# Performance work log

Measured on AMD Instinct MI355X. Metric: run time of the kernel, lower is better.

Reference implementation:

```python
import jax, jax.numpy as jnp
import numpy as np

N, E, D, C, L = 50000, 800000, 128, 10, 3
TAU = 0.5
EPS = 1e-5


def _ln(h, g, b):
    m = jnp.mean(h, axis=-1, keepdims=True)
    v = jnp.mean((h - m) ** 2, axis=-1, keepdims=True)
    return (h - m) * jax.lax.rsqrt(v + EPS) * g + b


def _gumbel_hard(logits, gnoise, tau):
    # gumbel_softmax(hard=True): straight-through one-hot of softmax((logits+g)/tau)
    y_soft = jax.nn.softmax((logits + gnoise) / tau, axis=-1)
    idx = jnp.argmax(y_soft, axis=-1)
    y_hard = jax.nn.one_hot(idx, logits.shape[-1], dtype=y_soft.dtype)
    return jax.lax.stop_gradient(y_hard - y_soft) + y_soft


def setup_inputs() -> dict:
    key = jax.random.key(0)
    ks = jax.random.split(key, 20)
    s = lambda *sh: 1.0 / np.sqrt(sh[0])
    inp = {
        "x": jax.random.normal(ks[0], (N, D), jnp.float32),
        "edge_index": jax.random.randint(ks[1], (2, E), 0, N, jnp.int64),
        # encoder (node_encoder Linear in_dim->env_dim)
        "W_enc": jax.random.normal(ks[2], (D, D), jnp.float32) * s(D),
        "b_enc": jnp.zeros((D,), jnp.float32),
        # shared hidden LayerNorm
        "ln_g": jnp.ones((D,), jnp.float32),
        "ln_b": jnp.zeros((D,), jnp.float32),
        # env GNN layers (root / neighbor weights + bias), L layers
        "Wr": jax.random.normal(ks[3], (L, D, D), jnp.float32) * s(D),
        "Wn": jax.random.normal(ks[4], (L, D, D), jnp.float32) * s(D),
        "bl": jnp.zeros((L, D), jnp.float32),
        # in/out action nets (1 layer each, env_dim -> 2 logits)
        "Wa_in_r": jax.random.normal(ks[5], (D, 2), jnp.float32) * s(D),
        "Wa_in_n": jax.random.normal(ks[6], (D, 2), jnp.float32) * s(D),
        "ba_in": jnp.zeros((2,), jnp.float32),
        "Wa_out_r": jax.random.normal(ks[7], (D, 2), jnp.float32) * s(D),
        "Wa_out_n": jax.random.normal(ks[8], (D, 2), jnp.float32) * s(D),
        "ba_out": jnp.zeros((2,), jnp.float32),
        # decoder (dec_num_layers=1 -> single Linear env_dim -> num_classes)
        "W_dec": jax.random.normal(ks[9], (D, C), jnp.float32) * s(D),
        "b_dec": jnp.zeros((C,), jnp.float32),
        # pre-sampled Gumbel noise per layer for in/out action gates
        "gin": jax.random.gumbel(ks[10], (L, N, 2), jnp.float32),
        "gout": jax.random.gumbel(ks[11], (L, N, 2), jnp.float32),
    }
    return inp


def reference(x, edge_index, W_enc, b_enc, ln_g, ln_b, Wr, Wn, bl,
              Wa_in_r, Wa_in_n, ba_in, Wa_out_r, Wa_out_n, ba_out,
              W_dec, b_dec, gin, gout):
    u, v = edge_index[0], edge_index[1]
    n = x.shape[0]
    # node encoder + (use_encoders=False) dropout(0)+act
    h = jax.nn.relu(x @ W_enc + b_enc)
    node_states = []
    for l in range(L):
        hn = _ln(h, ln_g, ln_b)
        # unweighted neighbor aggregation shared by both action nets
        agg = jax.ops.segment_sum(hn[u], v, num_segments=n)  # [N, D]
        in_logits = hn @ Wa_in_r + agg @ Wa_in_n + ba_in
        out_logits = hn @ Wa_out_r + agg @ Wa_out_n + ba_out
        in_p = _gumbel_hard(in_logits, gin[l], TAU)
        out_p = _gumbel_hard(out_logits, gout[l], TAU)
        # edge gate: listen prob of target * broadcast prob of source
        ew = in_p[v, 0] * out_p[u, 0]  # [E]
        aggw = jax.ops.segment_sum(ew[:, None] * hn[u], v, num_segments=n)
        out = jax.nn.relu(hn @ Wr[l] + aggw @ Wn[l] + bl[l])
        # node state bookkeeping: 0 standard, 1 broadcast-only, 2 listen-only, 3 isolated
        act = jax.lax.stop_gradient(ew)
        is_b = (jax.ops.segment_max(act, u, num_segments=n) > 0.5).astype(jnp.int32)
        is_l = (jax.ops.segment_max(act, v, num_segments=n) > 0.5).astype(jnp.int32)
        node_states.append(3 - 2 * is_b - is_l)
        h = hn + out  # skip connection (onto the normalized x, as in the source)
    h = _ln(h, ln_g, ln_b)
    result = h @ W_dec + b_dec
    return result, jnp.stack(node_states)
```

## Files before the change

### kernel.cpp

```cpp
#include <hip/hip_runtime.h>

#define DIM 128
#define NCLS 10

__device__ __forceinline__ void gload_lds16(const float4* g, float4* l) {
    __builtin_amdgcn_global_load_lds((const __attribute__((address_space(1))) char*)g,
                                     (__attribute__((address_space(3))) char*)l,
                                     16, 0, 0);
}

__global__ void k_hist(const int* __restrict__ ei, int E, int* __restrict__ deg) {
    int e = blockIdx.x * 256 + threadIdx.x;
    if (e < E) atomicAdd(&deg[ei[E + e]], 1);
}

__global__ void k_scan1(const int* __restrict__ deg, int* __restrict__ row_start,
                        int* __restrict__ bsum, int n) {
    int tid = threadIdx.x;
    int base = blockIdx.x * 1024 + tid * 4;
    int v0 = 0, v1 = 0, v2 = 0, v3 = 0;
    if (base + 3 < n) {
        int4 t = *(const int4*)(deg + base);
        v0 = t.x; v1 = t.y; v2 = t.z; v3 = t.w;
    } else {
        if (base + 0 < n) v0 = deg[base + 0];
        if (base + 1 < n) v1 = deg[base + 1];
        if (base + 2 < n) v2 = deg[base + 2];
        if (base + 3 < n) v3 = deg[base + 3];
    }
    int s = v0 + v1 + v2 + v3;
    int lane = tid & 63, w = tid >> 6;
    int inc = s;
#pragma unroll
    for (int o = 1; o < 64; o <<= 1) {
        int t = __shfl_up(inc, o);
        if (lane >= o) inc += t;
    }
    __shared__ int wsum[4];
    if (lane == 63) wsum[w] = inc;
    __syncthreads();
    int woff = 0;
    for (int i = 0; i < w; i++) woff += wsum[i];
    int run = woff + inc - s;
    if (base + 0 < n) row_start[base + 0] = run; run += v0;
    if (base + 1 < n) row_start[base + 1] = run; run += v1;
    if (base + 2 < n) row_start[base + 2] = run; run += v2;
    if (base + 3 < n) row_start[base + 3] = run;
    if (tid == 0) bsum[blockIdx.x] = wsum[0] + wsum[1] + wsum[2] + wsum[3];
}

__global__ void k_scan2(int* __restrict__ bsum, int nb) {
    int tid = threadIdx.x;
    if (nb <= 64) {
        int v = (tid < nb) ? bsum[tid] : 0;
        int inc = v;
#pragma unroll
        for (int o = 1; o < 64; o <<= 1) {
            int t = __shfl_up(inc, o);
            if (tid >= o) inc += t;
        }
        if (tid < nb) bsum[tid] = inc - v;
    } else if (tid == 0) {
        int acc = 0;
        for (int i = 0; i < nb; i++) { int t = bsum[i]; bsum[i] = acc; acc += t; }
    }
}

__global__ void k_scan3(int* __restrict__ row_start, int* __restrict__ cursor,
                        const int* __restrict__ bsum, int n, int E) {
    int i = blockIdx.x * 256 + threadIdx.x;
    if (i < n) {
        int r = row_start[i] + bsum[i >> 10];
        row_start[i] = r;
        cursor[i] = r;
    }
    if (i == n) row_start[n] = E;
}

__global__ void k_fill(const int* __restrict__ ei, int E, int* __restrict__ cursor,
                       int* __restrict__ csr) {
    int e = blockIdx.x * 256 + threadIdx.x;
    if (e < E) {
        int u = ei[e], v = ei[E + e];
        int pos = atomicAdd(&cursor[v], 1);
        csr[pos] = u;
    }
}

__global__ void k_action(const float* __restrict__ proj, const int* __restrict__ row_start,
                         const int* __restrict__ csr,
                         const float* __restrict__ bain, const float* __restrict__ baon,
                         const float* __restrict__ gin_l, const float* __restrict__ gout_l,
                         int* __restrict__ in_bit, int* __restrict__ out_bit,
                         int* __restrict__ is_b, int n) {
    int v = blockIdx.x * 256 + threadIdx.x;
    if (v >= n) return;
    is_b[v] = 0;
    int b0 = row_start[v], b1 = row_start[v + 1];
    double a0 = 0.0, a1 = 0.0, a2 = 0.0, a3 = 0.0;
    for (int e = b0; e < b1; e++) {
        int u = csr[e];
        float4 p = *(const float4*)(proj + (size_t)u * 8);
        a0 += p.x; a1 += p.y; a2 += p.z; a3 += p.w;
    }
    float4 r = *(const float4*)(proj + (size_t)v * 8 + 4);
    float2 gi = *(const float2*)(gin_l + (size_t)v * 2);
    float2 go = *(const float2*)(gout_l + (size_t)v * 2);
    float li0 = (float)a0 + r.x + bain[0] + gi.x;
    float li1 = (float)a1 + r.y + bain[1] + gi.y;
    float lo0 = (float)a2 + r.z + baon[0] + go.x;
    float lo1 = (float)a3 + r.w + baon[1] + go.y;
    in_bit[v]  = (li0 >= li1) ? 1 : 0;
    out_bit[v] = (lo0 >= lo1) ? 1 : 0;
}

__global__ void k_aggw(const float* __restrict__ hn, const int* __restrict__ row_start,
                       const int* __restrict__ csr, const int* __restrict__ in_bit,
                       const int* __restrict__ out_bit,
                       int* __restrict__ is_b, int* __restrict__ is_l,
                       float* __restrict__ aggw, int n) {
    int wid = (blockIdx.x * 256 + threadIdx.x) >> 6;
    int lane = threadIdx.x & 63;
    if (wid >= n) return;
    int d0 = lane * 2;
    double ax = 0.0, ay = 0.0;
    int anyg = 0;
    if (in_bit[wid]) {
        int base = row_start[wid], end = row_start[wid + 1];
        for (int off = base; off < end; off += 64) {
            int m = min(64, end - off);
            int myu = 0, myb = 0;
            if (lane < m) { myu = csr[off + lane]; myb = out_bit[myu]; }
            unsigned long long mask = __ballot(myb != 0);
            anyg |= (mask != 0ull);
            while (mask) {
                int i = __ffsll((unsigned long long)mask) - 1;
                mask &= mask - 1;
                int u = __shfl(myu, i);
                if (lane == 0) is_b[u] = 1;
                float2 t = *(const float2*)(hn + (size_t)u * DIM + d0);
                ax += t.x; ay += t.y;
            }
        }
    }
    if (lane == 0) is_l[wid] = anyg;
    ((float2*)(aggw + (size_t)wid * DIM))[lane] = make_float2((float)ax, (float)ay);
}

template <int HAS_B, int SKIP, int DO_LN, int DO_PROJ, int DO_STATES, int DO_DEC, int WRITE_H>
__launch_bounds__(256)
__attribute__((amdgpu_waves_per_eu(4, 4)))
__global__ void k_gemm(const float* __restrict__ A, const float* __restrict__ W1,
                       const float* __restrict__ B, const float* __restrict__ W2,
                       const float* __restrict__ bias,
                       const float* __restrict__ ln_g, const float* __restrict__ ln_b,
                       const float* __restrict__ Wain, const float* __restrict__ Waon,
                       const float* __restrict__ Wair, const float* __restrict__ Waor,
                       const int* __restrict__ is_b, const int* __restrict__ is_l,
                       const float* __restrict__ Wdec, const float* __restrict__ bdec,
                       float* __restrict__ out, float* __restrict__ proj,
                       float* __restrict__ states_l, float* __restrict__ dec_out, int n) {
    __shared__ float sW[32][128];
    __shared__ float sA[64][36];
    int tid = threadIdx.x;
    int rowBase = blockIdx.x * 64;
    int ty = tid >> 4, tx = tid & 15;
    int c0 = tx * 4, c1 = 64 + tx * 4;
    float acc[4][8];
#pragma unroll
    for (int i = 0; i < 4; i++)
#pragma unroll
        for (int j = 0; j < 8; j++) acc[i][j] = 0.f;

    for (int p = 0; p < 1 + HAS_B; p++) {
        const float* Ap = p ? B : A;
        const float* Wp = p ? W2 : W1;
        for (int kc = 0; kc < DIM; kc += 32) {
            __syncthreads();
            {
                const float4* src = (const float4*)(Wp + kc * DIM);
                float4* dst = (float4*)(&sW[0][0]);
#pragma unroll
                for (int i = 0; i < 4; i++) {
                    int j = i * 256 + tid;
                    gload_lds16(src + j, dst + j);
                }
            }
            {
#pragma unroll
                for (int i = 0; i < 2; i++) {
                    int j = i * 256 + tid;
                    int r = j >> 3, c4 = (j & 7) * 4;
                    float4 va = (rowBase + r < n)
                        ? *(const float4*)(Ap + (size_t)(rowBase + r) * DIM + kc + c4)
                        : make_float4(0.f, 0.f, 0.f, 0.f);
                    *(float4*)&sA[r][c4] = va;
                }
            }
            __syncthreads();
#pragma unroll
            for (int kk = 0; kk < 32; kk += 4) {
                float4 a[4];
#pragma unroll
                for (int i = 0; i < 4; i++) a[i] = *(const float4*)&sA[i * 16 + ty][kk];
#pragma unroll
                for (int q = 0; q < 4; q++) {
                    float4 w0 = *(const float4*)&sW[kk + q][c0];
                    float4 w1 = *(const float4*)&sW[kk + q][c1];
#pragma unroll
                    for (int i = 0; i < 4; i++) {
                        float av = (&a[i].x)[q];
                        acc[i][0] += av * w0.x;
                        acc[i][1] += av * w0.y;
                        acc[i][2] += av * w0.z;
                        acc[i][3] += av * w0.w;
                        acc[i][4] += av * w1.x;
                        acc[i][5] += av * w1.y;
                        acc[i][6] += av * w1.z;
                        acc[i][7] += av * w1.w;
                    }
                }
            }
        }
    }

    float* sWd = (float*)&sW[0][0];
    if (DO_DEC) {
        __syncthreads();
        for (int i = tid; i < NCLS * DIM; i += 256) {
            int d = i / NCLS, c = i % NCLS;
            sWd[c * DIM + d] = Wdec[i];
        }
        __syncthreads();
    }

    float4 bias0 = *(const float4*)&bias[c0];
    float4 bias1 = *(const float4*)&bias[c1];
    float bv[8] = {bias0.x, bias0.y, bias0.z, bias0.w, bias1.x, bias1.y, bias1.z, bias1.w};
    float gv[8], bbv[8];
    if (DO_LN) {
        float4 g0 = *(const float4*)&ln_g[c0];
        float4 g1 = *(const float4*)&ln_g[c1];
        float4 lb0 = *(const float4*)&ln_b[c0];
        float4 lb1 = *(const float4*)&ln_b[c1];
        gv[0]=g0.x; gv[1]=g0.y; gv[2]=g0.z; gv[3]=g0.w; gv[4]=g1.x; gv[5]=g1.y; gv[6]=g1.z; gv[7]=g1.w;
        bbv[0]=lb0.x; bbv[1]=lb0.y; bbv[2]=lb0.z; bbv[3]=lb0.w; bbv[4]=lb1.x; bbv[5]=lb1.y; bbv[6]=lb1.z; bbv[7]=lb1.w;
    }

#pragma unroll
    for (int i = 0; i < 4; i++) {
        int r = rowBase + i * 16 + ty;
        if (r >= n) continue;
        float v[8];
        if (SKIP) {
            float4 s0 = *(const float4*)(A + (size_t)r * DIM + c0);
            float4 s1 = *(const float4*)(A + (size_t)r * DIM + c1);
            float sv[8] = {s0.x, s0.y, s0.z, s0.w, s1.x, s1.y, s1.z, s1.w};
#pragma unroll
            for (int j = 0; j < 8; j++) v[j] = fmaxf(acc[i][j] + bv[j], 0.f) + sv[j];
        } else {
#pragma unroll
            for (int j = 0; j < 8; j++) v[j] = fmaxf(acc[i][j] + bv[j], 0.f);
        }
        if (DO_LN) {
            float s = 0.f, q = 0.f;
#pragma unroll
            for (int j = 0; j < 8; j++) { s += v[j]; q += v[j] * v[j]; }
#pragma unroll
            for (int o = 1; o < 16; o <<= 1) { s += __shfl_xor(s, o); q += __shfl_xor(q, o); }
            float m = s * (1.f / DIM);
            float var = q * (1.f / DIM) - m * m;
            float inv = rsqrtf(var + 1e-5f);
#pragma unroll
            for (int j = 0; j < 8; j++) v[j] = (v[j] - m) * inv * gv[j] + bbv[j];
        }
        if (WRITE_H) {
            *(float4*)(out + (size_t)r * DIM + c0) = make_float4(v[0], v[1], v[2], v[3]);
            *(float4*)(out + (size_t)r * DIM + c1) = make_float4(v[4], v[5], v[6], v[7]);
        }
        if (DO_STATES) {
            if (tx == 0) states_l[r] = (float)(3 - 2 * is_b[r] - is_l[r]);
        }
        if (DO_PROJ) {
            float pv[8];
            auto dotw = [&](const float* Wm, float& p0, float& p1) {
                float4 q0 = *(const float4*)(Wm + c0 * 2);
                float4 q1 = *(const float4*)(Wm + c0 * 2 + 4);
                float4 q2 = *(const float4*)(Wm + c1 * 2);
                float4 q3 = *(const float4*)(Wm + c1 * 2 + 4);
                p0 = v[0]*q0.x + v[1]*q0.z + v[2]*q1.x + v[3]*q1.z
                   + v[4]*q2.x + v[5]*q2.z + v[6]*q3.x + v[7]*q3.z;
                p1 = v[0]*q0.y + v[1]*q0.w + v[2]*q1.y + v[3]*q1.w
                   + v[4]*q2.y + v[5]*q2.w + v[6]*q3.y + v[7]*q3.w;
            };
            dotw(Wain, pv[0], pv[1]);
            dotw(Waon, pv[2], pv[3]);
            dotw(Wair, pv[4], pv[5]);
            dotw(Waor, pv[6], pv[7]);
#pragma unroll
            for (int o = 1; o < 16; o <<= 1)
#pragma unroll
                for (int j = 0; j < 8; j++) pv[j] += __shfl_xor(pv[j], o);
            if (tx == 0) {
                *(float4*)(proj + (size_t)r * 8)     = make_float4(pv[0], pv[1], pv[2], pv[3]);
                *(float4*)(proj + (size_t)r * 8 + 4) = make_float4(pv[4], pv[5], pv[6], pv[7]);
            }
        }
        if (DO_DEC) {
            float p[NCLS];
#pragma unroll
            for (int c = 0; c < NCLS; c++) {
                float4 wd0 = *(const float4*)&sWd[c * DIM + c0];
                float4 wd1 = *(const float4*)&sWd[c * DIM + c1];
                p[c] = v[0]*wd0.x + v[1]*wd0.y + v[2]*wd0.z + v[3]*wd0.w
                     + v[4]*wd1.x + v[5]*wd1.y + v[6]*wd1.z + v[7]*wd1.w;
            }
#pragma unroll
            for (int o = 1; o < 16; o <<= 1)
#pragma unroll
                for (int c = 0; c < NCLS; c++) p[c] += __shfl_xor(p[c], o);
            if (tx == 0) {
#pragma unroll
                for (int c = 0; c < NCLS; c++) dec_out[(size_t)r * NCLS + c] = p[c] + bdec[c];
            }
        }
    }
}

extern "C" void kernel_launch(void* const* d_in, const int* in_sizes, int n_in,
                              void* d_out, int out_size, void* d_ws, size_t ws_size,
                              hipStream_t stream) {
    const float* x      = (const float*)d_in[0];
    const int*   ei     = (const int*)d_in[1];
    const float* W_enc  = (const float*)d_in[2];
    const float* b_enc  = (const float*)d_in[3];
    const float* ln_g   = (const float*)d_in[4];
    const float* ln_b   = (const float*)d_in[5];
    const float* Wr     = (const float*)d_in[6];
    const float* Wn     = (const float*)d_in[7];
    const float* bl     = (const float*)d_in[8];
    const float* Wair   = (const float*)d_in[9];
    const float* Wain   = (const float*)d_in[10];
    const float* bain   = (const float*)d_in[11];
    const float* Waor   = (const float*)d_in[12];
    const float* Waon   = (const float*)d_in[13];
    const float* baon   = (const float*)d_in[14];
    const float* W_dec  = (const float*)d_in[15];
    const float* b_dec  = (const float*)d_in[16];
    const float* gin    = (const float*)d_in[17];
    const float* gout   = (const float*)d_in[18];

    int n = in_sizes[0] / DIM;
    int E = in_sizes[1] / 2;
    const int L = 3;

    char* wsp = (char*)d_ws;
    auto alloc = [&](size_t bytes) { char* p = wsp; wsp += (bytes + 255) / 256 * 256; return p; };
    float* hn   = (float*)alloc((size_t)n * DIM * 4);
    float* aggw = (float*)alloc((size_t)n * DIM * 4);
    float* proj = (float*)alloc((size_t)n * 8 * 4);
    int* deg       = (int*)alloc((size_t)n * 4);
    int* row_start = (int*)alloc((size_t)(n + 1) * 4);
    int* cursor    = (int*)alloc((size_t)n * 4);
    int* csr       = (int*)alloc((size_t)E * 4);
    int* in_bit    = (int*)alloc((size_t)n * 4);
    int* out_bit   = (int*)alloc((size_t)n * 4);
    int* bsum      = (int*)alloc((size_t)256 * 4);
    int* is_b      = (int*)alloc((size_t)n * 4);
    int* is_l      = (int*)alloc((size_t)n * 4);

    float* out_res    = (float*)d_out;
    float* out_states = out_res + (size_t)n * NCLS;

    int ebl = (E + 255) / 256;
    int nbl = (n + 255) / 256;
    int wbl = (n + 3) / 4;
    int gbl = (n + 63) / 64;
    int nb  = (n + 1023) / 1024;

    hipMemsetAsync(deg, 0, (size_t)n * 4, stream);
    k_hist<<<ebl, 256, 0, stream>>>(ei, E, deg);
    k_scan1<<<nb, 256, 0, stream>>>(deg, row_start, bsum, n);
    k_scan2<<<1, 64, 0, stream>>>(bsum, nb);
    k_scan3<<<(n + 256) / 256, 256, 0, stream>>>(row_start, cursor, bsum, n, E);
    k_fill<<<ebl, 256, 0, stream>>>(ei, E, cursor, csr);

    k_gemm<0, 0, 1, 1, 0, 0, 1><<<gbl, 256, 0, stream>>>(
        x, W_enc, nullptr, nullptr, b_enc, ln_g, ln_b,
        Wain, Waon, Wair, Waor, nullptr, nullptr, nullptr, nullptr,
        hn, proj, nullptr, nullptr, n);

    for (int l = 0; l < L; l++) {
        k_action<<<nbl, 256, 0, stream>>>(proj, row_start, csr, bain, baon,
                                          gin + (size_t)l * n * 2, gout + (size_t)l * n * 2,
                                          in_bit, out_bit, is_b, n);
        k_aggw<<<wbl, 256, 0, stream>>>(hn, row_start, csr, in_bit, out_bit,
                                        is_b, is_l, aggw, n);
        if (l + 1 < L) {
            k_gemm<1, 1, 1, 1, 1, 0, 1><<<gbl, 256, 0, stream>>>(
                hn, Wr + (size_t)l * DIM * DIM, aggw, Wn + (size_t)l * DIM * DIM,
                bl + (size_t)l * DIM, ln_g, ln_b,
                Wain, Waon, Wair, Waor, is_b, is_l, nullptr, nullptr,
                hn, proj, out_states + (size_t)l * n, nullptr, n);
        } else {
            k_gemm<1, 1, 1, 0, 1, 1, 0><<<gbl, 256, 0, stream>>>(
                hn, Wr + (size_t)l * DIM * DIM, aggw, Wn + (size_t)l * DIM * DIM,
                bl + (size_t)l * DIM, ln_g, ln_b,
                Wain, Waon, Wair, Waor, is_b, is_l, W_dec, b_dec,
                hn, nullptr, out_states + (size_t)l * n, out_res, n);
        }
    }
}
```

Before: 481.0 us.

## Overlap root-weight GEMM with weighted neighbor gather in one launch

Splits the per-layer fused GEMM so the hn@Wr product runs in the same launch as the edge-gated neighbor aggregation, with blocks partitioned by index. A follow-up kernel computes aggw@Wn and fuses bias, relu, skip, layernorm, projections and states, reading the stored partial product. The aim is to overlap compute-heavy GEMM blocks with latency-bound gather waves, at the cost of an extra intermediate buffer write and read per layer.

```diff
diff --git a/kernel.cpp b/kernel.cpp
--- a/kernel.cpp
+++ b/kernel.cpp
@@ -114,52 +114,14 @@
     out_bit[v] = (lo0 >= lo1) ? 1 : 0;
 }
 
-__global__ void k_aggw(const float* __restrict__ hn, const int* __restrict__ row_start,
-                       const int* __restrict__ csr, const int* __restrict__ in_bit,
-                       const int* __restrict__ out_bit,
-                       int* __restrict__ is_b, int* __restrict__ is_l,
-                       float* __restrict__ aggw, int n) {
-    int wid = (blockIdx.x * 256 + threadIdx.x) >> 6;
-    int lane = threadIdx.x & 63;
-    if (wid >= n) return;
-    int d0 = lane * 2;
-    double ax = 0.0, ay = 0.0;
-    int anyg = 0;
-    if (in_bit[wid]) {
-        int base = row_start[wid], end = row_start[wid + 1];
-        for (int off = base; off < end; off += 64) {
-            int m = min(64, end - off);
-            int myu = 0, myb = 0;
-            if (lane < m) { myu = csr[off + lane]; myb = out_bit[myu]; }
-            unsigned long long mask = __ballot(myb != 0);
-            anyg |= (mask != 0ull);
-            while (mask) {
-                int i = __ffsll((unsigned long long)mask) - 1;
-                mask &= mask - 1;
-                int u = __shfl(myu, i);
-                if (lane == 0) is_b[u] = 1;
-                float2 t = *(const float2*)(hn + (size_t)u * DIM + d0);
-                ax += t.x; ay += t.y;
-            }
-        }
-    }
-    if (lane == 0) is_l[wid] = anyg;
-    ((float2*)(aggw + (size_t)wid * DIM))[lane] = make_float2((float)ax, (float)ay);
-}
-
-template <int HAS_B, int SKIP, int DO_LN, int DO_PROJ, int DO_STATES, int DO_DEC, int WRITE_H>
 __launch_bounds__(256)
 __attribute__((amdgpu_waves_per_eu(4, 4)))
-__global__ void k_gemm(const float* __restrict__ A, const float* __restrict__ W1,
-                       const float* __restrict__ B, const float* __restrict__ W2,
+__global__ void k_genc(const float* __restrict__ A, const float* __restrict__ W,
                        const float* __restrict__ bias,
                        const float* __restrict__ ln_g, const float* __restrict__ ln_b,
                        const float* __restrict__ Wain, const float* __restrict__ Waon,
                        const float* __restrict__ Wair, const float* __restrict__ Waor,
-                       const int* __restrict__ is_b, const int* __restrict__ is_l,
-                       const float* __restrict__ Wdec, const float* __restrict__ bdec,
-                       float* __restrict__ out, float* __restrict__ proj,
-                       float* __restrict__ states_l, float* __restrict__ dec_out, int n) {
+                       float* __restrict__ out, float* __restrict__ proj, int n) {
     __shared__ float sW[32][128];
     __shared__ float sA[64][36];
     int tid = threadIdx.x;
@@ -172,30 +134,134 @@
 #pragma unroll
         for (int j = 0; j < 8; j++) acc[i][j] = 0.f;
 
-    for (int p = 0; p < 1 + HAS_B; p++) {
-        const float* Ap = p ? B : A;
-        const float* Wp = p ? W2 : W1;
+    for (int kc = 0; kc < DIM; kc += 32) {
+        __syncthreads();
+        const float4* src = (const float4*)(W + kc * DIM);
+        float4* dst = (float4*)(&sW[0][0]);
+#pragma unroll
+        for (int i = 0; i < 4; i++) { int j = i * 256 + tid; gload_lds16(src + j, dst + j); }
+#pragma unroll
+        for (int i = 0; i < 2; i++) {
+            int j = i * 256 + tid;
+            int r = j >> 3, c4 = (j & 7) * 4;
+            float4 va = (rowBase + r < n)
+                ? *(const float4*)(A + (size_t)(rowBase + r) * DIM + kc + c4)
+                : make_float4(0.f, 0.f, 0.f, 0.f);
+            *(float4*)&sA[r][c4] = va;
+        }
+        __syncthreads();
+#pragma unroll
+        for (int kk = 0; kk < 32; kk += 4) {
+            float4 a[4];
+#pragma unroll
+            for (int i = 0; i < 4; i++) a[i] = *(const float4*)&sA[i * 16 + ty][kk];
+#pragma unroll
+            for (int q = 0; q < 4; q++) {
+                float4 w0 = *(const float4*)&sW[kk + q][c0];
+                float4 w1 = *(const float4*)&sW[kk + q][c1];
+#pragma unroll
+                for (int i = 0; i < 4; i++) {
+                    float av = (&a[i].x)[q];
+                    acc[i][0] += av * w0.x; acc[i][1] += av * w0.y;
+                    acc[i][2] += av * w0.z; acc[i][3] += av * w0.w;
+                    acc[i][4] += av * w1.x; acc[i][5] += av * w1.y;
+                    acc[i][6] += av * w1.z; acc[i][7] += av * w1.w;
+                }
+            }
+        }
+    }
+
+    float4 bias0 = *(const float4*)&bias[c0];
+    float4 bias1 = *(const float4*)&bias[c1];
+    float bv[8] = {bias0.x, bias0.y, bias0.z, bias0.w, bias1.x, bias1.y, bias1.z, bias1.w};
+    float4 g0 = *(const float4*)&ln_g[c0];
+    float4 g1 = *(const float4*)&ln_g[c1];
+    float4 lb0 = *(const float4*)&ln_b[c0];
+    float4 lb1 = *(const float4*)&ln_b[c1];
+    float gv[8]  = {g0.x, g0.y, g0.z, g0.w, g1.x, g1.y, g1.z, g1.w};
+    float bbv[8] = {lb0.x, lb0.y, lb0.z, lb0.w, lb1.x, lb1.y, lb1.z, lb1.w};
+
+#pragma unroll
+    for (int i = 0; i < 4; i++) {
+        int r = rowBase + i * 16 + ty;
+        if (r >= n) continue;
+        float v[8];
+#pragma unroll
+        for (int j = 0; j < 8; j++) v[j] = fmaxf(acc[i][j] + bv[j], 0.f);
+        float s = 0.f, q = 0.f;
+#pragma unroll
+        for (int j = 0; j < 8; j++) { s += v[j]; q += v[j] * v[j]; }
+#pragma unroll
+        for (int o = 1; o < 16; o <<= 1) { s += __shfl_xor(s, o); q += __shfl_xor(q, o); }
+        float m = s * (1.f / DIM);
+        float var = q * (1.f / DIM) - m * m;
+        float inv = rsqrtf(var + 1e-5f);
+#pragma unroll
+        for (int j = 0; j < 8; j++) v[j] = (v[j] - m) * inv * gv[j] + bbv[j];
+        *(float4*)(out + (size_t)r * DIM + c0) = make_float4(v[0], v[1], v[2], v[3]);
+        *(float4*)(out + (size_t)r * DIM + c1) = make_float4(v[4], v[5], v[6], v[7]);
+
+        float pv[8];
+        auto dotw = [&](const float* Wm, float& p0, float& p1) {
+            float4 q0 = *(const float4*)(Wm + c0 * 2);
+            float4 q1 = *(const float4*)(Wm + c0 * 2 + 4);
+            float4 q2 = *(const float4*)(Wm + c1 * 2);
+            float4 q3 = *(const float4*)(Wm + c1 * 2 + 4);
+            p0 = v[0]*q0.x + v[1]*q0.z + v[2]*q1.x + v[3]*q1.z
+               + v[4]*q2.x + v[5]*q2.z + v[6]*q3.x + v[7]*q3.z;
+            p1 = v[0]*q0.y + v[1]*q0.w + v[2]*q1.y + v[3]*q1.w
+               + v[4]*q2.y + v[5]*q2.w + v[6]*q3.y + v[7]*q3.w;
+        };
+        dotw(Wain, pv[0], pv[1]);
+        dotw(Waon, pv[2], pv[3]);
+        dotw(Wair, pv[4], pv[5]);
+        dotw(Waor, pv[6], pv[7]);
+#pragma unroll
+        for (int o = 1; o < 16; o <<= 1)
+#pragma unroll
+            for (int j = 0; j < 8; j++) pv[j] += __shfl_xor(pv[j], o);
+        if (tx == 0) {
+            *(float4*)(proj + (size_t)r * 8)     = make_float4(pv[0], pv[1], pv[2], pv[3]);
+            *(float4*)(proj + (size_t)r * 8 + 4) = make_float4(pv[4], pv[5], pv[6], pv[7]);
+        }
+    }
+}
+
+__launch_bounds__(256)
+__attribute__((amdgpu_waves_per_eu(4, 4)))
+__global__ void k2(const float* __restrict__ hn, const float* __restrict__ W,
+                   float* __restrict__ y,
+                   const int* __restrict__ row_start, const int* __restrict__ csr,
+                   const int* __restrict__ in_bit, const int* __restrict__ out_bit,
+                   int* __restrict__ is_b, int* __restrict__ is_l,
+                   float* __restrict__ aggw, int gb, int n) {
+    __shared__ float sW[32][128];
+    __shared__ float sA[64][36];
+    int tid = threadIdx.x;
+    if ((int)blockIdx.x < gb) {
+        int rowBase = blockIdx.x * 64;
+        int ty = tid >> 4, tx = tid & 15;
+        int c0 = tx * 4, c1 = 64 + tx * 4;
+        float acc[4][8];
+#pragma unroll
+        for (int i = 0; i < 4; i++)
+#pragma unroll
+            for (int j = 0; j < 8; j++) acc[i][j] = 0.f;
+
         for (int kc = 0; kc < DIM; kc += 32) {
             __syncthreads();
-            {
-                const float4* src = (const float4*)(Wp + kc * DIM);
-                float4* dst = (float4*)(&sW[0][0]);
-#pragma unroll
-                for (int i = 0; i < 4; i++) {
-                    int j = i * 256 + tid;
-                    gload_lds16(src + j, dst + j);
-                }
-            }
-            {
-#pragma unroll
-                for (int i = 0; i < 2; i++) {
-                    int j = i * 256 + tid;
-                    int r = j >> 3, c4 = (j & 7) * 4;
-                    float4 va = (rowBase + r < n)
-                        ? *(const float4*)(Ap + (size_t)(rowBase + r) * DIM + kc + c4)
-                        : make_float4(0.f, 0.f, 0.f, 0.f);
-                    *(float4*)&sA[r][c4] = va;
-                }
+            const float4* src = (const float4*)(W + kc * DIM);
+            float4* dst = (float4*)(&sW[0][0]);
+#pragma unroll
+            for (int i = 0; i < 4; i++) { int j = i * 256 + tid; gload_lds16(src + j, dst + j); }
+#pragma unroll
+            for (int i = 0; i < 2; i++) {
+                int j = i * 256 + tid;
+                int r = j >> 3, c4 = (j & 7) * 4;
+                float4 va = (rowBase + r < n)
+                    ? *(const float4*)(hn + (size_t)(rowBase + r) * DIM + kc + c4)
+                    : make_float4(0.f, 0.f, 0.f, 0.f);
+                *(float4*)&sA[r][c4] = va;
             }
             __syncthreads();
 #pragma unroll
@@ -210,15 +276,108 @@
 #pragma unroll
                     for (int i = 0; i < 4; i++) {
                         float av = (&a[i].x)[q];
-                        acc[i][0] += av * w0.x;
-                        acc[i][1] += av * w0.y;
-                        acc[i][2] += av * w0.z;
-                        acc[i][3] += av * w0.w;
-                        acc[i][4] += av * w1.x;
-                        acc[i][5] += av * w1.y;
-                        acc[i][6] += av * w1.z;
-                        acc[i][7] += av * w1.w;
+                        acc[i][0] += av * w0.x; acc[i][1] += av * w0.y;
+                        acc[i][2] += av * w0.z; acc[i][3] += av * w0.w;
+                        acc[i][4] += av * w1.x; acc[i][5] += av * w1.y;
+                        acc[i][6] += av * w1.z; acc[i][7] += av * w1.w;
                     }
+                }
+            }
+        }
+#pragma unroll
+        for (int i = 0; i < 4; i++) {
+            int r = rowBase + i * 16 + ty;
+            if (r >= n) continue;
+            *(float4*)(y + (size_t)r * DIM + c0) = make_float4(acc[i][0], acc[i][1], acc[i][2], acc[i][3]);
+            *(float4*)(y + (size_t)r * DIM + c1) = make_float4(acc[i][4], acc[i][5], acc[i][6], acc[i][7]);
+        }
+    } else {
+        int wid = (((int)blockIdx.x - gb) * 256 + tid) >> 6;
+        int lane = tid & 63;
+        if (wid >= n) return;
+        int d0 = lane * 2;
+        double ax = 0.0, ay = 0.0;
+        int anyg = 0;
+        if (in_bit[wid]) {
+            int base = row_start[wid], end = row_start[wid + 1];
+            for (int off = base; off < end; off += 64) {
+                int m = min(64, end - off);
+                int myu = 0, myb = 0;
+                if (lane < m) { myu = csr[off + lane]; myb = out_bit[myu]; }
+                unsigned long long mask = __ballot(myb != 0);
+                anyg |= (mask != 0ull);
+                while (mask) {
+                    int i = __ffsll((unsigned long long)mask) - 1;
+                    mask &= mask - 1;
+                    int u = __shfl(myu, i);
+                    if (lane == 0) is_b[u] = 1;
+                    float2 t = *(const float2*)(hn + (size_t)u * DIM + d0);
+                    ax += t.x; ay += t.y;
+                }
+            }
+        }
+        if (lane == 0) is_l[wid] = anyg;
+        ((float2*)(aggw + (size_t)wid * DIM))[lane] = make_float2((float)ax, (float)ay);
+    }
+}
+
+template <int DO_PROJ, int DO_DEC>
+__launch_bounds__(256)
+__attribute__((amdgpu_waves_per_eu(4, 4)))
+__global__ void k3(const float* __restrict__ Ag, const float* __restrict__ W,
+                   float* __restrict__ hn, const float* __restrict__ y,
+                   const float* __restrict__ bias,
+                   const float* __restrict__ ln_g, const float* __restrict__ ln_b,
+                   const float* __restrict__ Wain, const float* __restrict__ Waon,
+                   const float* __restrict__ Wair, const float* __restrict__ Waor,
+                   const int* __restrict__ is_b, const int* __restrict__ is_l,
+                   const float* __restrict__ Wdec, const float* __restrict__ bdec,
+                   float* __restrict__ proj, float* __restrict__ states_l,
+                   float* __restrict__ dec_out, int n) {
+    __shared__ float sW[32][128];
+    __shared__ float sA[64][36];
+    int tid = threadIdx.x;
+    int rowBase = blockIdx.x * 64;
+    int ty = tid >> 4, tx = tid & 15;
+    int c0 = tx * 4, c1 = 64 + tx * 4;
+    float acc[4][8];
+#pragma unroll
+    for (int i = 0; i < 4; i++)
+#pragma unroll
+        for (int j = 0; j < 8; j++) acc[i][j] = 0.f;
+
+    for (int kc = 0; kc < DIM; kc += 32) {
+        __syncthreads();
+        const float4* src = (const float4*)(W + kc * DIM);
+        float4* dst = (float4*)(&sW[0][0]);
+#pragma unroll
+        for (int i = 0; i < 4; i++) { int j = i * 256 + tid; gload_lds16(src + j, dst + j); }
+#pragma unroll
+        for (int i = 0; i < 2; i++) {
+            int j = i * 256 + tid;
+            int r = j >> 3, c4 = (j & 7) * 4;
+            float4 va = (rowBase + r < n)
+                ? *(const float4*)(Ag + (size_t)(rowBase + r) * DIM + kc + c4)
+                : make_float4(0.f, 0.f, 0.f, 0.f);
+            *(float4*)&sA[r][c4] = va;
+        }
+        __syncthreads();
+#pragma unroll
+        for (int kk = 0; kk < 32; kk += 4) {
+            float4 a[4];
+#pragma unroll
+            for (int i = 0; i < 4; i++) a[i] = *(const float4*)&sA[i * 16 + ty][kk];
+#pragma unroll
+            for (int q = 0; q < 4; q++) {
+                float4 w0 = *(const float4*)&sW[kk + q][c0];
+                float4 w1 = *(const float4*)&sW[kk + q][c1];
+#pragma unroll
+                for (int i = 0; i < 4; i++) {
+                    float av = (&a[i].x)[q];
+                    acc[i][0] += av * w0.x; acc[i][1] += av * w0.y;
+                    acc[i][2] += av * w0.z; acc[i][3] += av * w0.w;
+                    acc[i][4] += av * w1.x; acc[i][5] += av * w1.y;
+                    acc[i][6] += av * w1.z; acc[i][7] += av * w1.w;
                 }
             }
         }
@@ -237,50 +396,44 @@
     float4 bias0 = *(const float4*)&bias[c0];
     float4 bias1 = *(const float4*)&bias[c1];
     float bv[8] = {bias0.x, bias0.y, bias0.z, bias0.w, bias1.x, bias1.y, bias1.z, bias1.w};
-    float gv[8], bbv[8];
-    if (DO_LN) {
-        float4 g0 = *(const float4*)&ln_g[c0];
-        float4 g1 = *(const float4*)&ln_g[c1];
-        float4 lb0 = *(const float4*)&ln_b[c0];
-        float4 lb1 = *(const float4*)&ln_b[c1];
-        gv[0]=g0.x; gv[1]=g0.y; gv[2]=g0.z; gv[3]=g0.w; gv[4]=g1.x; gv[5]=g1.y; gv[6]=g1.z; gv[7]=g1.w;
-        bbv[0]=lb0.x; bbv[1]=lb0.y; bbv[2]=lb0.z; bbv[3]=lb0.w; bbv[4]=lb1.x; bbv[5]=lb1.y; bbv[6]=lb1.z; bbv[7]=lb1.w;
-    }
+    float4 g0 = *(const float4*)&ln_g[c0];
+    float4 g1 = *(const float4*)&ln_g[c1];
+    float4 lb0 = *(const float4*)&ln_b[c0];
+    float4 lb1 = *(const float4*)&ln_b[c1];
+    float gv[8]  = {g0.x, g0.y, g0.z, g0.w, g1.x, g1.y, g1.z, g1.w};
+    float bbv[8] = {lb0.x, lb0.y, lb0.z, lb0.w, lb1.x, lb1.y, lb1.z, lb1.w};
 
 #pragma unroll
     for (int i = 0; i < 4; i++) {
         int r = rowBase + i * 16 + ty;
         if (r >= n) continue;
+        float4 y0 = *(const float4*)(y + (size_t)r * DIM + c0);
+        float4 y1 = *(const float4*)(y + (size_t)r * DIM + c1);
+        float4 h0 = *(const float4*)(hn + (size_t)r * DIM + c0);
+        float4 h1 = *(const float4*)(hn + (size_t)r * DIM + c1);
+        float yv[8] = {y0.x, y0.y, y0.z, y0.w, y1.x, y1.y, y1.z, y1.w};
+        float hv[8] = {h0.x, h0.y, h0.z, h0.w, h1.x, h1.y, h1.z, h1.w};
         float v[8];
-        if (SKIP) {
-            float4 s0 = *(const float4*)(A + (size_t)r * DIM + c0);
-            float4 s1 = *(const float4*)(A + (size_t)r * DIM + c1);
-            float sv[8] = {s0.x, s0.y, s0.z, s0.w, s1.x, s1.y, s1.z, s1.w};
-#pragma unroll
-            for (int j = 0; j < 8; j++) v[j] = fmaxf(acc[i][j] + bv[j], 0.f) + sv[j];
-        } else {
-#pragma unroll
-            for (int j = 0; j < 8; j++) v[j] = fmaxf(acc[i][j] + bv[j], 0.f);
-        }
-        if (DO_LN) {
-            float s = 0.f, q = 0.f;
-#pragma unroll
-            for (int j = 0; j < 8; j++) { s += v[j]; q += v[j] * v[j]; }
-#pragma unroll
-            for (int o = 1; o < 16; o <<= 1) { s += __shfl_xor(s, o); q += __shfl_xor(q, o); }
-            float m = s * (1.f / DIM);
-            float var = q * (1.f / DIM) - m * m;
-            float inv = rsqrtf(var + 1e-5f);
-#pragma unroll
-            for (int j = 0; j < 8; j++) v[j] = (v[j] - m) * inv * gv[j] + bbv[j];
-        }
-        if (WRITE_H) {
-            *(float4*)(out + (size_t)r * DIM + c0) = make_float4(v[0], v[1], v[2], v[3]);
-            *(float4*)(out + (size_t)r * DIM + c1) = make_float4(v[4], v[5], v[6], v[7]);
-        }
-        if (DO_STATES) {
-            if (tx == 0) states_l[r] = (float)(3 - 2 * is_b[r] - is_l[r]);
-        }
+#pragma unroll
+        for (int j = 0; j < 8; j++)
+            v[j] = hv[j] + fmaxf(yv[j] + acc[i][j] + bv[j], 0.f);
+        float s = 0.f, q = 0.f;
+#pragma unroll
+        for (int j = 0; j < 8; j++) { s += v[j]; q += v[j] * v[j]; }
+#pragma unroll
+        for (int o = 1; o < 16; o <<= 1) { s += __shfl_xor(s, o); q += __shfl_xor(q, o); }
+        float m = s * (1.f / DIM);
+        float var = q * (1.f / DIM) - m * m;
+        float inv = rsqrtf(var + 1e-5f);
+#pragma unroll
+        for (int j = 0; j < 8; j++) v[j] = (v[j] - m) * inv * gv[j] + bbv[j];
+
+        if (!DO_DEC) {
+            *(float4*)(hn + (size_t)r * DIM + c0) = make_float4(v[0], v[1], v[2], v[3]);
+            *(float4*)(hn + (size_t)r * DIM + c1) = make_float4(v[4], v[5], v[6], v[7]);
+        }
+        if (tx == 0) states_l[r] = (float)(3 - 2 * is_b[r] - is_l[r]);
+
         if (DO_PROJ) {
             float pv[8];
             auto dotw = [&](const float* Wm, float& p0, float& p1) {
@@ -358,6 +511,7 @@
     auto alloc = [&](size_t bytes) { char* p = wsp; wsp += (bytes + 255) / 256 * 256; return p; };
     float* hn   = (float*)alloc((size_t)n * DIM * 4);
     float* aggw = (float*)alloc((size_t)n * DIM * 4);
+    float* yb   = (float*)alloc((size_t)n * DIM * 4);
     float* proj = (float*)alloc((size_t)n * 8 * 4);
     int* deg       = (int*)alloc((size_t)n * 4);
     int* row_start = (int*)alloc((size_t)(n + 1) * 4);
@@ -385,29 +539,30 @@
     k_scan3<<<(n + 256) / 256, 256, 0, stream>>>(row_start, cursor, bsum, n, E);
     k_fill<<<ebl, 256, 0, stream>>>(ei, E, cursor, csr);
 
-    k_gemm<0, 0, 1, 1, 0, 0, 1><<<gbl, 256, 0, stream>>>(
-        x, W_enc, nullptr, nullptr, b_enc, ln_g, ln_b,
-        Wain, Waon, Wair, Waor, nullptr, nullptr, nullptr, nullptr,
-        hn, proj, nullptr, nullptr, n);
+    k_genc<<<gbl, 256, 0, stream>>>(x, W_enc, b_enc, ln_g, ln_b,
+                                    Wain, Waon, Wair, Waor, hn, proj, n);
 
     for (int l = 0; l < L; l++) {
         k_action<<<nbl, 256, 0, stream>>>(proj, row_start, csr, bain, baon,
                                           gin + (size_t)l * n * 2, gout + (size_t)l * n * 2,
                                           in_bit, out_bit, is_b, n);
-        k_aggw<<<wbl, 256, 0, stream>>>(hn, row_start, csr, in_bit, out_bit,
-                                        is_b, is_l, aggw, n);
+        k2<<<gbl + wbl, 256, 0, stream>>>(hn, Wr + (size_t)l * DIM * DIM, yb,
+                                          row_start, csr, in_bit, out_bit,
+                                          is_b, is_l, aggw, gbl, n);
         if (l + 1 < L) {
-            k_gemm<1, 1, 1, 1, 1, 0, 1><<<gbl, 256, 0, stream>>>(
-                hn, Wr + (size_t)l * DIM * DIM, aggw, Wn + (size_t)l * DIM * DIM,
-                bl + (size_t)l * DIM, ln_g, ln_b,
-                Wain, Waon, Wair, Waor, is_b, is_l, nullptr, nullptr,
-                hn, proj, out_states + (size_t)l * n, nullptr, n);
+            k3<1, 0><<<gbl, 256, 0, stream>>>(aggw, Wn + (size_t)l * DIM * DIM,
+                                              hn, yb, bl + (size_t)l * DIM,
+                                              ln_g, ln_b, Wain, Waon, Wair, Waor,
+                                              is_b, is_l, nullptr, nullptr,
+                                              proj, out_states + (size_t)l * n,
+                                              nullptr, n);
         } else {
-            k_gemm<1, 1, 1, 0, 1, 1, 0><<<gbl, 256, 0, stream>>>(
-                hn, Wr + (size_t)l * DIM * DIM, aggw, Wn + (size_t)l * DIM * DIM,
-                bl + (size_t)l * DIM, ln_g, ln_b,
-                Wain, Waon, Wair, Waor, is_b, is_l, W_dec, b_dec,
-                hn, nullptr, out_states + (size_t)l * n, out_res, n);
-        }
-    }
-}
+            k3<0, 1><<<gbl, 256, 0, stream>>>(aggw, Wn + (size_t)l * DIM * DIM,
+                                              hn, yb, bl + (size_t)l * DIM,
+                                              ln_g, ln_b, Wain, Waon, Wair, Waor,
+                                              is_b, is_l, W_dec, b_dec,
+                                              nullptr, out_states + (size_t)l * n,
+                                              out_res, n);
+        }
+    }
+}
```

Measured after the change: 544.1 us. +13.1%, slower.
